# Kernel optimization log

Measured on AMD Instinct MI355X. Metric: run time of the kernel, lower is better.

## Reference

```python
import jax, jax.numpy as jnp
from jax import lax
import numpy as np

OBJECT_W, BCE_W, DICE_W = 2.0, 5.0, 5.0
B, N, M, C = 8, 128, 32, 65536


def setup_inputs() -> dict:
    key = jax.random.key(0)
    k1, k2, k3 = jax.random.split(key, 3)
    objectness = jax.random.normal(k1, (B, N), jnp.float32)
    pred_masks = jax.random.normal(k2, (B, N, C), jnp.float32)
    gt_masks = jax.random.randint(k3, (B, M, C), 0, 2).astype(jnp.float32)
    return {"objectness": objectness, "pred_masks": pred_masks, "gt_masks": gt_masks}


def _cost_matrices(objectness, pred, gt):
    # BCE-with-logits vs all-ones target: log(1+exp(-x)) = softplus(-x)
    # BCE-with-logits vs all-zeros target: softplus(x)
    sp_pos = jax.nn.softplus(-pred)                       # [B,N,C]
    sp_neg = jax.nn.softplus(pred)                        # [B,N,C]
    # einsum('nc,mc->nm', pos, t) + einsum('nc,mc->nm', neg, 1-t), batched.
    # neg @ (1-t) = neg.sum(c) - neg @ t (avoids materializing 1-t).
    bce = (jnp.einsum('bnc,bmc->bnm', sp_pos, gt)
           + sp_neg.sum(-1)[:, :, None]
           - jnp.einsum('bnc,bmc->bnm', sp_neg, gt)) / pred.shape[-1]
    s = jax.nn.sigmoid(pred)
    numerator = 2.0 * jnp.einsum('bnc,bmc->bnm', s, gt)
    denominator = s.sum(-1)[:, :, None] + gt.sum(-1)[:, None, :]
    dice = 1.0 - (numerator + 1.0) / (denominator + 1.0)
    obj = -jax.nn.sigmoid(objectness)[:, :, None]         # [B,N,1]
    return OBJECT_W * obj + BCE_W * bce + DICE_W * dice    # [B,N,M]


def _lsap(cost):
    """Jonker-Volgenant shortest-augmenting-path LSAP (scipy algorithm).
    cost: [R, C] with R <= C. Returns col4row [R] int32: column per row."""
    R, Cn = cost.shape
    BIG = jnp.float32(1e30)

    def outer(cur_row, carry):
        u, v, row4col, col4row = carry
        shortest = jnp.full((Cn,), BIG, jnp.float32)
        path = jnp.full((Cn,), -1, jnp.int32)
        SR = jnp.zeros((R,), bool)
        SC = jnp.zeros((Cn,), bool)

        def sp_cond(s):
            return s[6] < 0

        def sp_body(s):
            i, shortest, path, SR, SC, minVal, sink = s
            SR = SR.at[i].set(True)
            d = minVal + cost[i] - u[i] - v
            better = (d < shortest) & (~SC)
            shortest = jnp.where(better, d, shortest)
            path = jnp.where(better, i, path)
            masked = jnp.where(SC, BIG, shortest)
            j = jnp.argmin(masked).astype(jnp.int32)
            minVal = masked[j]
            SC = SC.at[j].set(True)
            nxt = row4col[j]
            sink = jnp.where(nxt == -1, j, jnp.int32(-1))
            i = jnp.where(nxt == -1, i, nxt)
            return (i, shortest, path, SR, SC, minVal, sink)

        init = (cur_row.astype(jnp.int32), shortest, path, SR, SC,
                jnp.float32(0.0), jnp.int32(-1))
        i, shortest, path, SR, SC, minVal, sink = lax.while_loop(sp_cond, sp_body, init)

        # dual updates (scipy rectangular_lsap)
        u = u.at[cur_row].add(minVal)
        extra = SR & (jnp.arange(R) != cur_row)
        sp_at_col = shortest[jnp.clip(col4row, 0, Cn - 1)]
        u = jnp.where(extra, u + minVal - sp_at_col, u)
        v = jnp.where(SC, v - (minVal - shortest), v)

        # augment along path
        def aug_cond(s):
            return ~s[3]

        def aug_body(s):
            j, row4col, col4row, done = s
            i = path[j]
            row4col = row4col.at[j].set(i)
            tmp = col4row[i]
            col4row = col4row.at[i].set(j)
            done = (i == cur_row)
            return (tmp, row4col, col4row, done)

        _, row4col, col4row, _ = lax.while_loop(
            aug_cond, aug_body, (sink, row4col, col4row, jnp.array(False)))
        return (u, v, row4col, col4row)

    carry = (jnp.zeros((R,), jnp.float32), jnp.zeros((Cn,), jnp.float32),
             jnp.full((Cn,), -1, jnp.int32), jnp.full((R,), -1, jnp.int32))
    u, v, row4col, col4row = lax.fori_loop(0, R, outer, carry)
    return col4row


def reference(objectness, pred_masks, gt_masks):
    cost = _cost_matrices(objectness, pred_masks, gt_masks)   # [B,N,M]
    # scipy lsap on [N,M] then sort by target == solving on cost.T [M,N]:
    # indices[b, m] = matched query index for target m.
    indices = jax.vmap(_lsap)(jnp.transpose(cost, (0, 2, 1)))  # [B,M]
    return cost, indices
```

## Files before the change

### kernel.cpp

```cpp
#include <hip/hip_runtime.h>
#include <hip/hip_bf16.h>

#define LOG2E 1.4426950408889634f
#define LN2   0.6931471805599453f

typedef __attribute__((ext_vector_type(8))) short short8;
typedef __attribute__((ext_vector_type(4))) float f32x4;

#define B_ 8
#define N_ 128
#define M_ 32
#define C_ 65536
#define KCHUNKS 64
#define KC (C_ / KCHUNKS)
#define BK 64
#define AST 72

__device__ __forceinline__ unsigned short f2bf(float f) {
  unsigned u = __builtin_bit_cast(unsigned, f);
  u += 0x7fffu + ((u >> 16) & 1u);
  return (unsigned short)(u >> 16);
}
__device__ __forceinline__ unsigned pack_rne(float lo, float hi) {
  return (unsigned)f2bf(lo) | ((unsigned)f2bf(hi) << 16);
}
__device__ __forceinline__ unsigned pack_trunc(float lo, float hi) {
  unsigned ul = __builtin_bit_cast(unsigned, lo);
  unsigned uh = __builtin_bit_cast(unsigned, hi);
  return (uh & 0xFFFF0000u) | (ul >> 16);
}

__global__ __launch_bounds__(256, 2) void cost_partial_kernel(
    const float* __restrict__ pred, const float* __restrict__ gt,
    float* __restrict__ xg_part, float* __restrict__ sg_part,
    float* __restrict__ sp_part, float* __restrict__ ss_part,
    float* __restrict__ gts_part)
{
  __shared__ unsigned short As[256 * AST];
  __shared__ unsigned short Bt[32 * AST];
  const int kc = blockIdx.x, b = blockIdx.y;
  const int tid = threadIdx.x;
  const int grp = tid >> 4, gl = tid & 15;
  const int grow = tid >> 3, gh = tid & 7;
  const int wave = tid >> 6, lane = tid & 63;
  const int quad = lane >> 4, lcol = lane & 15;
  const int c0 = kc * KC;
  const int slab = kc * B_ + b;

  const float* predB = pred + (size_t)b * N_ * C_ + c0;
  const float* gtB   = gt   + (size_t)b * M_ * C_ + (size_t)grow * C_ + c0;

  float spr[8], sr[8], gtacc = 0.f;
#pragma unroll
  for (int r = 0; r < 8; ++r) { spr[r] = 0.f; sr[r] = 0.f; }

  f32x4 acc[4][2];
#pragma unroll
  for (int rt = 0; rt < 4; ++rt)
#pragma unroll
    for (int ct = 0; ct < 2; ++ct)
      acc[rt][ct] = (f32x4){0.f, 0.f, 0.f, 0.f};

  for (int ks = 0; ks < KC / BK; ++ks) {
    const int cb = ks * BK;
    float4 p[8];
#pragma unroll
    for (int r = 0; r < 8; ++r)
      p[r] = *(const float4*)(predB + (size_t)(r * 16 + grp) * C_ + cb + gl * 4);
    float4 g0 = *(const float4*)(gtB + cb + gh * 4);
    float4 g1 = *(const float4*)(gtB + cb + (gh + 8) * 4);

#pragma unroll
    for (int r = 0; r < 8; ++r) {
      const int row = r * 16 + grp;
      float xs[4] = {p[r].x, p[r].y, p[r].z, p[r].w};
      float ss[4];
#pragma unroll
      for (int e = 0; e < 4; ++e) {
        float x = xs[e];
        float t = fminf(fmaxf(x * LOG2E, -80.f), 80.f);
        float e2 = __builtin_amdgcn_exp2f(t);
        float z = 1.f + e2;
        float s = e2 * __builtin_amdgcn_rcpf(z);
        spr[r] += __builtin_amdgcn_logf(z) * LN2;
        sr[r]  += s;
        ss[e] = s;
      }
      *(uint2*)&As[row * AST + gl * 4] =
          (uint2){pack_rne(xs[0], xs[1]), pack_rne(xs[2], xs[3])};
      *(uint2*)&As[(N_ + row) * AST + gl * 4] =
          (uint2){pack_rne(ss[0], ss[1]), pack_rne(ss[2], ss[3])};
    }
    gtacc += g0.x + g0.y + g0.z + g0.w + g1.x + g1.y + g1.z + g1.w;
    *(uint2*)&Bt[grow * AST + gh * 4] =
        (uint2){pack_trunc(g0.x, g0.y), pack_trunc(g0.z, g0.w)};
    *(uint2*)&Bt[grow * AST + (gh + 8) * 4] =
        (uint2){pack_trunc(g1.x, g1.y), pack_trunc(g1.z, g1.w)};
    __syncthreads();

#pragma unroll
    for (int k0 = 0; k0 < BK; k0 += 32) {
      const int koff = k0 + quad * 8;
      short8 bf0 = *(const short8*)&Bt[lcol * AST + koff];
      short8 bf1 = *(const short8*)&Bt[(16 + lcol) * AST + koff];
#pragma unroll
      for (int rt = 0; rt < 4; ++rt) {
        short8 af = *(const short8*)&As[(wave * 64 + rt * 16 + lcol) * AST + koff];
        acc[rt][0] = __builtin_amdgcn_mfma_f32_16x16x32_bf16(af, bf0, acc[rt][0], 0, 0, 0);
        acc[rt][1] = __builtin_amdgcn_mfma_f32_16x16x32_bf16(af, bf1, acc[rt][1], 0, 0, 0);
      }
    }
    __syncthreads();
  }

#pragma unroll
  for (int r = 0; r < 8; ++r) {
    float v1 = spr[r], v2 = sr[r];
#pragma unroll
    for (int off = 1; off < 16; off <<= 1) {
      v1 += __shfl_xor(v1, off);
      v2 += __shfl_xor(v2, off);
    }
    if (gl == 0) {
      sp_part[slab * N_ + r * 16 + grp] = v1;
      ss_part[slab * N_ + r * 16 + grp] = v2;
    }
  }
  gtacc += __shfl_xor(gtacc, 1);
  gtacc += __shfl_xor(gtacc, 2);
  gtacc += __shfl_xor(gtacc, 4);
  if (gh == 0) gts_part[slab * M_ + grow] = gtacc;

#pragma unroll
  for (int rt = 0; rt < 4; ++rt)
#pragma unroll
    for (int ct = 0; ct < 2; ++ct)
#pragma unroll
      for (int reg = 0; reg < 4; ++reg) {
        int orow = wave * 64 + rt * 16 + quad * 4 + reg;
        int ocol = ct * 16 + lcol;
        float v = acc[rt][ct][reg];
        if (orow < N_) xg_part[(slab * N_ + orow) * M_ + ocol] = v;
        else           sg_part[(slab * N_ + (orow - N_)) * M_ + ocol] = v;
      }
}

__global__ void finalize_kernel(const float* __restrict__ obj,
    const float* __restrict__ xg_part, const float* __restrict__ sg_part,
    const float* __restrict__ sp_part, const float* __restrict__ ss_part,
    const float* __restrict__ gts_part, float* __restrict__ cost)
{
  int idx = blockIdx.x * blockDim.x + threadIdx.x;
  int b = idx >> 12;
  int n = (idx >> 5) & 127;
  int m = idx & 31;
  float xa = 0.f, sa = 0.f, spa = 0.f, ssa = 0.f, ga = 0.f;
#pragma unroll 4
  for (int kc = 0; kc < KCHUNKS; ++kc) {
    int slab = kc * B_ + b;
    xa  += xg_part[(slab * N_ + n) * M_ + m];
    sa  += sg_part[(slab * N_ + n) * M_ + m];
    spa += sp_part[slab * N_ + n];
    ssa += ss_part[slab * N_ + n];
    ga  += gts_part[slab * M_ + m];
  }
  float o = obj[b * N_ + n];
  float t = fminf(fmaxf(o * LOG2E, -80.f), 80.f);
  float e2 = __builtin_amdgcn_exp2f(t);
  float sig = e2 * __builtin_amdgcn_rcpf(1.f + e2);
  float bce = (spa - xa) * (1.0f / (float)C_);
  float dice = 1.f - (2.f * sa + 1.f) / (ssa + ga + 1.f);
  cost[idx] = -2.f * sig + 5.f * bce + 5.f * dice;
}

#define BIGF 1e30f

__device__ __forceinline__ float wave_min_all(float x) {
  const int BI = __builtin_bit_cast(int, BIGF);
  int v = __builtin_bit_cast(int, x);
#define MIN_STEP(ctrl)                                                        \
  {                                                                           \
    int t_ = __builtin_amdgcn_update_dpp(BI, v, ctrl, 0xf, 0xf, false);       \
    v = __builtin_bit_cast(int, fminf(__builtin_bit_cast(float, v),           \
                                      __builtin_bit_cast(float, t_)));        \
  }
  MIN_STEP(0x111)
  MIN_STEP(0x112)
  MIN_STEP(0x114)
  MIN_STEP(0x118)
  MIN_STEP(0x142)
  MIN_STEP(0x143)
#undef MIN_STEP
  return __builtin_bit_cast(float, __builtin_amdgcn_readlane(v, 63));
}

__device__ __forceinline__ float rdlane_f(float x, int l) {
  return __builtin_bit_cast(float, __builtin_amdgcn_readlane(__builtin_bit_cast(int, x), l));
}

__global__ __launch_bounds__(64) void lsap_kernel(const float* __restrict__ cost,
                                                  float* __restrict__ out)
{
  const int b = blockIdx.x;
  const int lane = threadIdx.x;
  __shared__ float cTs[M_ * 129];

#pragma unroll 4
  for (int t = 0; t < 16; ++t) {
    int e = t * 256 + lane * 4;
    float4 v4 = *(const float4*)&cost[b * 4096 + e];
    int n = e >> 5, m = e & 31;
    cTs[(m + 0) * 129 + n] = v4.x;
    cTs[(m + 1) * 129 + n] = v4.y;
    cTs[(m + 2) * 129 + n] = v4.z;
    cTs[(m + 3) * 129 + n] = v4.w;
  }
  __syncthreads();

  float u_reg = 0.f;
  int c4r = -1;
  float v0 = 0.f, v1 = 0.f;
  int r40 = -1, r41 = -1;

  for (int cur = 0; cur < M_; ++cur) {
    float sh0 = BIGF, sh1 = BIGF;
    int p0 = -1, p1 = -1;
    bool sc0 = false, sc1 = false;
    unsigned srmask = 0u;
    int i = cur, sink = -1;
    float minVal = 0.f;

    while (sink < 0) {
      srmask |= 1u << i;
      float ui = rdlane_f(u_reg, i);
      float cc0 = cTs[i * 129 + 2 * lane];
      float cc1 = cTs[i * 129 + 2 * lane + 1];
      float d0 = ((minVal + cc0) - ui) - v0;
      float d1 = ((minVal + cc1) - ui) - v1;
      if (!sc0 && d0 < sh0) { sh0 = d0; p0 = i; }
      if (!sc1 && d1 < sh1) { sh1 = d1; p1 = i; }
      float m0 = sc0 ? BIGF : sh0;
      float m1 = sc1 ? BIGF : sh1;
      float mv = wave_min_all(fminf(m0, m1));
      unsigned long long bl0 = __ballot(m0 == mv);
      unsigned long long bl1 = __ballot(m1 == mv);
      int j0 = bl0 ? 2 * (int)__builtin_ctzll(bl0) : 0x7fffffff;
      int j1 = bl1 ? 2 * (int)__builtin_ctzll(bl1) + 1 : 0x7fffffff;
      int j = j0 < j1 ? j0 : j1;
      minVal = mv;
      if (lane == (j >> 1)) { if (j & 1) sc1 = true; else sc0 = true; }
      int nxt = __builtin_amdgcn_readlane((j & 1) ? r41 : r40, j >> 1);
      if (nxt < 0) sink = j; else i = nxt;
    }

    int jj = c4r < 0 ? 0 : c4r;
    float g0 = __shfl(sh0, jj >> 1);
    float g1 = __shfl(sh1, jj >> 1);
    float sj = (jj & 1) ? g1 : g0;
    if (lane < M_) {
      if (lane == cur) u_reg += minVal;
      else if ((srmask >> lane) & 1u) u_reg += minVal - sj;
    }
    if (sc0) v0 -= minVal - sh0;
    if (sc1) v1 -= minVal - sh1;

    int j = sink;
    while (true) {
      int i2 = __builtin_amdgcn_readlane((j & 1) ? p1 : p0, j >> 1);
      if (lane == (j >> 1)) { if (j & 1) r41 = i2; else r40 = i2; }
      int tmp = __builtin_amdgcn_readlane(c4r, i2);
      if (lane == i2) c4r = j;
      if (i2 == cur) break;
      j = tmp;
    }
  }
  if (lane < M_) out[b * M_ + lane] = (float)c4r;
}

extern "C" void kernel_launch(void* const* d_in, const int* in_sizes, int n_in,
                              void* d_out, int out_size, void* d_ws, size_t ws_size,
                              hipStream_t stream)
{
  const float* obj  = (const float*)d_in[0];
  const float* pred = (const float*)d_in[1];
  const float* gt   = (const float*)d_in[2];
  float* out = (float*)d_out;

  float* xg_part  = (float*)d_ws;
  float* sg_part  = xg_part + (size_t)KCHUNKS * B_ * N_ * M_;
  float* sp_part  = sg_part + (size_t)KCHUNKS * B_ * N_ * M_;
  float* ss_part  = sp_part + (size_t)KCHUNKS * B_ * N_;
  float* gts_part = ss_part + (size_t)KCHUNKS * B_ * N_;

  cost_partial_kernel<<<dim3(KCHUNKS, B_), 256, 0, stream>>>(
      pred, gt, xg_part, sg_part, sp_part, ss_part, gts_part);
  finalize_kernel<<<dim3(32768 / 256), 256, 0, stream>>>(
      obj, xg_part, sg_part, sp_part, ss_part, gts_part, out);
  lsap_kernel<<<dim3(B_), 64, 0, stream>>>(out, out + 32768);
}
```

Baseline: 569.7 us.

## Prefetch next k-tile into registers, trim softplus math, use native bf16 convert

The main cost kernel now loads the next 64-column slice of pred and gt into registers while the current slice is converted and fed to MFMA, so global load latency can overlap with compute. The per-element ln2 multiply moves out of the inner loop to the final reduction, the lower clamp on the exp2 argument is dropped, and the hand-written bf16 packing is replaced with the library conversion. The finalize kernel switches to 64-thread blocks. The register prefetch doubles the live input registers, which may reduce occupancy under the two-blocks-per-SM launch bound.

```diff
diff --git a/kernel.cpp b/kernel.cpp
--- a/kernel.cpp
+++ b/kernel.cpp
@@ -16,18 +16,11 @@
 #define BK 64
 #define AST 72
 
-__device__ __forceinline__ unsigned short f2bf(float f) {
-  unsigned u = __builtin_bit_cast(unsigned, f);
-  u += 0x7fffu + ((u >> 16) & 1u);
-  return (unsigned short)(u >> 16);
-}
-__device__ __forceinline__ unsigned pack_rne(float lo, float hi) {
-  return (unsigned)f2bf(lo) | ((unsigned)f2bf(hi) << 16);
-}
-__device__ __forceinline__ unsigned pack_trunc(float lo, float hi) {
-  unsigned ul = __builtin_bit_cast(unsigned, lo);
-  unsigned uh = __builtin_bit_cast(unsigned, hi);
-  return (uh & 0xFFFF0000u) | (ul >> 16);
+__device__ __forceinline__ unsigned pack2(float lo, float hi) {
+  union { __hip_bfloat16 h; unsigned short s; } a, b;
+  a.h = __float2bfloat16(lo);
+  b.h = __float2bfloat16(hi);
+  return (unsigned)a.s | ((unsigned)b.s << 16);
 }
 
 __global__ __launch_bounds__(256, 2) void cost_partial_kernel(
@@ -61,14 +54,23 @@
     for (int ct = 0; ct < 2; ++ct)
       acc[rt][ct] = (f32x4){0.f, 0.f, 0.f, 0.f};
 
+  float4 p[8], g0, g1;
+#pragma unroll
+  for (int r = 0; r < 8; ++r)
+    p[r] = *(const float4*)(predB + (size_t)(r * 16 + grp) * C_ + gl * 4);
+  g0 = *(const float4*)(gtB + gh * 4);
+  g1 = *(const float4*)(gtB + (gh + 8) * 4);
+
   for (int ks = 0; ks < KC / BK; ++ks) {
-    const int cb = ks * BK;
-    float4 p[8];
-#pragma unroll
-    for (int r = 0; r < 8; ++r)
-      p[r] = *(const float4*)(predB + (size_t)(r * 16 + grp) * C_ + cb + gl * 4);
-    float4 g0 = *(const float4*)(gtB + cb + gh * 4);
-    float4 g1 = *(const float4*)(gtB + cb + (gh + 8) * 4);
+    float4 pn[8], gn0, gn1;
+    if (ks + 1 < KC / BK) {
+      const int cb = (ks + 1) * BK;
+#pragma unroll
+      for (int r = 0; r < 8; ++r)
+        pn[r] = *(const float4*)(predB + (size_t)(r * 16 + grp) * C_ + cb + gl * 4);
+      gn0 = *(const float4*)(gtB + cb + gh * 4);
+      gn1 = *(const float4*)(gtB + cb + (gh + 8) * 4);
+    }
 
 #pragma unroll
     for (int r = 0; r < 8; ++r) {
@@ -78,24 +80,24 @@
 #pragma unroll
       for (int e = 0; e < 4; ++e) {
         float x = xs[e];
-        float t = fminf(fmaxf(x * LOG2E, -80.f), 80.f);
+        float t = fminf(x * LOG2E, 80.f);
         float e2 = __builtin_amdgcn_exp2f(t);
         float z = 1.f + e2;
         float s = e2 * __builtin_amdgcn_rcpf(z);
-        spr[r] += __builtin_amdgcn_logf(z) * LN2;
+        spr[r] += __builtin_amdgcn_logf(z);
         sr[r]  += s;
         ss[e] = s;
       }
       *(uint2*)&As[row * AST + gl * 4] =
-          (uint2){pack_rne(xs[0], xs[1]), pack_rne(xs[2], xs[3])};
+          (uint2){pack2(xs[0], xs[1]), pack2(xs[2], xs[3])};
       *(uint2*)&As[(N_ + row) * AST + gl * 4] =
-          (uint2){pack_rne(ss[0], ss[1]), pack_rne(ss[2], ss[3])};
+          (uint2){pack2(ss[0], ss[1]), pack2(ss[2], ss[3])};
     }
     gtacc += g0.x + g0.y + g0.z + g0.w + g1.x + g1.y + g1.z + g1.w;
     *(uint2*)&Bt[grow * AST + gh * 4] =
-        (uint2){pack_trunc(g0.x, g0.y), pack_trunc(g0.z, g0.w)};
+        (uint2){pack2(g0.x, g0.y), pack2(g0.z, g0.w)};
     *(uint2*)&Bt[grow * AST + (gh + 8) * 4] =
-        (uint2){pack_trunc(g1.x, g1.y), pack_trunc(g1.z, g1.w)};
+        (uint2){pack2(g1.x, g1.y), pack2(g1.z, g1.w)};
     __syncthreads();
 
 #pragma unroll
@@ -111,6 +113,12 @@
       }
     }
     __syncthreads();
+
+    if (ks + 1 < KC / BK) {
+#pragma unroll
+      for (int r = 0; r < 8; ++r) p[r] = pn[r];
+      g0 = gn0; g1 = gn1;
+    }
   }
 
 #pragma unroll
@@ -122,7 +130,7 @@
       v2 += __shfl_xor(v2, off);
     }
     if (gl == 0) {
-      sp_part[slab * N_ + r * 16 + grp] = v1;
+      sp_part[slab * N_ + r * 16 + grp] = v1 * LN2;
       ss_part[slab * N_ + r * 16 + grp] = v2;
     }
   }
@@ -165,7 +173,7 @@
     ga  += gts_part[slab * M_ + m];
   }
   float o = obj[b * N_ + n];
-  float t = fminf(fmaxf(o * LOG2E, -80.f), 80.f);
+  float t = fminf(o * LOG2E, 80.f);
   float e2 = __builtin_amdgcn_exp2f(t);
   float sig = e2 * __builtin_amdgcn_rcpf(1.f + e2);
   float bce = (spa - xa) * (1.0f / (float)C_);
@@ -294,7 +302,7 @@
 
   cost_partial_kernel<<<dim3(KCHUNKS, B_), 256, 0, stream>>>(
       pred, gt, xg_part, sg_part, sp_part, ss_part, gts_part);
-  finalize_kernel<<<dim3(32768 / 256), 256, 0, stream>>>(
+  finalize_kernel<<<dim3(32768 / 64), 64, 0, stream>>>(
       obj, xg_part, sg_part, sp_part, ss_part, gts_part, out);
   lsap_kernel<<<dim3(B_), 64, 0, stream>>>(out, out + 32768);
 }
```

Result: no change. 571.2 us (+0.3%).
